# Kernel optimization log

Hardware: AMD Instinct MI355X
Metric: run time of the kernel (lower is better)

## Reference

```python
import jax, jax.numpy as jnp
import numpy as np

# 1x1 conv (bias=False) + BatchNorm (eval mode, running mean=0, var=1 -> per-channel
# affine scale/shift, matching SyncBN at init/inference) + ReLU
def _cbr(x, W, g, b):
    y = jnp.einsum('bchw,oc->bohw', x, W)
    y = y * g[None, :, None, None] + b[None, :, None, None]
    return jax.nn.relu(y)


def setup_inputs() -> dict:
    key = jax.random.key(0)
    ks = jax.random.split(key, 8)
    B, C, H, Wd = 4, 512, 64, 64   # batch, feats_channels, spatial
    Ct = 256                        # transform_channels
    Ck = 2 * C                      # key_in_channels = feats_channels * 2

    def w(k, o, i):
        return jax.random.normal(k, (o, i), jnp.float32) * (1.0 / np.sqrt(i))

    inp = {"x": jax.random.normal(ks[0], (B, C, H, Wd), jnp.float32)}
    # query_project: two conv+BN+ReLU blocks, C -> Ct -> Ct
    inp["qW1"] = w(ks[1], Ct, C);  inp["qg1"] = jnp.ones((Ct,), jnp.float32); inp["qb1"] = jnp.zeros((Ct,), jnp.float32)
    inp["qW2"] = w(ks[2], Ct, Ct); inp["qg2"] = jnp.ones((Ct,), jnp.float32); inp["qb2"] = jnp.zeros((Ct,), jnp.float32)
    # key_project: two conv+BN+ReLU blocks, 2C -> Ct -> Ct
    inp["kW1"] = w(ks[3], Ct, Ck); inp["kg1"] = jnp.ones((Ct,), jnp.float32); inp["kb1"] = jnp.zeros((Ct,), jnp.float32)
    inp["kW2"] = w(ks[4], Ct, Ct); inp["kg2"] = jnp.ones((Ct,), jnp.float32); inp["kb2"] = jnp.zeros((Ct,), jnp.float32)
    # value_project: one conv+BN+ReLU, 2C -> Ct
    inp["vW"] = w(ks[5], Ct, Ck);  inp["vg"] = jnp.ones((Ct,), jnp.float32);  inp["vb"] = jnp.zeros((Ct,), jnp.float32)
    # out_project: one conv+BN+ReLU, Ct -> C
    inp["oW"] = w(ks[6], C, Ct);   inp["og"] = jnp.ones((C,), jnp.float32);   inp["ob"] = jnp.zeros((C,), jnp.float32)
    return inp


def reference(x, qW1, qg1, qb1, qW2, qg2, qb2,
              kW1, kg1, kb1, kW2, kg2, kb2,
              vW, vg, vb, oW, og, ob):
    B, C, H, W = x.shape
    # global avgpool to 1x1, bilinear-upsample back to HxW == broadcast of the mean
    xg = jnp.broadcast_to(jnp.mean(x, axis=(2, 3), keepdims=True), (B, C, H, W))
    key_feats = jnp.concatenate([xg, x], axis=1)  # [B, 2C, H, W]

    q = _cbr(_cbr(x, qW1, qg1, qb1), qW2, qg2, qb2)          # [B, Ct, H, W]
    k = _cbr(_cbr(key_feats, kW1, kg1, kb1), kW2, kg2, kb2)  # [B, Ct, H, W]
    v = _cbr(key_feats, vW, vg, vb)                          # [B, Ct, H, W]

    Ct = q.shape[1]
    HW = H * W
    qf = q.reshape(B, Ct, HW).transpose(0, 2, 1)  # [B, HW, Ct]
    kf = k.reshape(B, Ct, HW)                     # [B, Ct, HW]
    vf = v.reshape(B, Ct, HW).transpose(0, 2, 1)  # [B, HW, Ct]

    sim = jnp.einsum('bnc,bcm->bnm', qf, kf) * (Ct ** -0.5)  # [B, HW, HW]
    attn = jax.nn.softmax(sim, axis=-1)
    ctx = jnp.einsum('bnm,bmc->bnc', attn, vf)               # [B, HW, Ct]
    ctx = ctx.transpose(0, 2, 1).reshape(B, Ct, H, W)

    return _cbr(ctx, oW, og, ob)  # [B, C, H, W]
```

## Files before the change

kernel.cpp:

```cpp
#include <hip/hip_runtime.h>
#include <stdint.h>

typedef __bf16 bf16x8 __attribute__((ext_vector_type(8)));
typedef float f32x4 __attribute__((ext_vector_type(4)));
typedef unsigned short u16;
typedef uint32_t u32;

union V16 { uint4 v; u16 e[8]; };

__device__ __forceinline__ float bf2f(u16 h) {
    u32 u = ((u32)h) << 16; float f; __builtin_memcpy(&f, &u, 4); return f;
}
__device__ __forceinline__ u16 f2bf(float f) {
    u32 u; __builtin_memcpy(&u, &f, 4);
    u32 r = (u + 0x7FFFu + ((u >> 16) & 1u)) >> 16; return (u16)r;
}
__device__ __forceinline__ u32 pack2(float a, float b) {
    return (u32)f2bf(a) | ((u32)f2bf(b) << 16);
}
__device__ __forceinline__ f32x4 mfma16(bf16x8 a, bf16x8 b, f32x4 c) {
    return __builtin_amdgcn_mfma_f32_16x16x32_bf16(a, b, c, 0, 0, 0);
}
__device__ __forceinline__ void gll16(const u16* g, u16* l) {
    __builtin_amdgcn_global_load_lds(
        (const __attribute__((address_space(1))) unsigned int*)g,
        (__attribute__((address_space(3))) unsigned int*)l, 16, 0, 0);
}
__device__ __forceinline__ float loadElem(const void* p, size_t i, int fl) {
    if (fl == 1) return ((const float*)p)[i];
    if (fl == 2) return (float)((const double*)p)[i];
    return bf2f(((const u16*)p)[i]);
}

__global__ __launch_bounds__(256) void k_detect(const u32* __restrict__ xw, int* __restrict__ flag) {
    int t = threadIdx.x;
    int cA = 0, cB = 0;
    #pragma unroll
    for (int i = 0; i < 16; i++) {
        u32 w = xw[i * 256 + t];
        cA += (((w >> 23) & 0xFFu) >= 0xC0u) ? 1 : 0;
        cB += (((w >> 7)  & 0xFFu) >= 0xC0u) ? 1 : 0;
    }
    #pragma unroll
    for (int m = 32; m >= 1; m >>= 1) { cA += __shfl_xor(cA, m); cB += __shfl_xor(cB, m); }
    __shared__ int sA[4], sB[4];
    if ((t & 63) == 0) { sA[t >> 6] = cA; sB[t >> 6] = cB; }
    __syncthreads();
    if (t == 0) {
        int a = sA[0] + sA[1] + sA[2] + sA[3];
        int b = sB[0] + sB[1] + sB[2] + sB[3];
        *flag = (a > 64) ? 2 : ((b > 64) ? 1 : 0);
    }
}

__global__ __launch_bounds__(256) void k_mean(const void* __restrict__ xv, const int* __restrict__ dt,
                                              float* __restrict__ xg) {
    int bc = blockIdx.x;
    int t = threadIdx.x;
    int fl = *dt;
    const size_t base = (size_t)bc * 4096;
    float s = 0.f;
    if (fl == 1) {
        const float* p = (const float*)xv + base;
        #pragma unroll
        for (int i = 0; i < 4; i++) {
            float4 v = *reinterpret_cast<const float4*>(p + (size_t)(i * 256 + t) * 4);
            s += v.x + v.y + v.z + v.w;
        }
    } else {
        for (int i = 0; i < 16; i++) s += loadElem(xv, base + i * 256 + t, fl);
    }
    #pragma unroll
    for (int m = 32; m >= 1; m >>= 1) s += __shfl_xor(s, m);
    __shared__ float wsum[4];
    if ((t & 63) == 0) wsum[t >> 6] = s;
    __syncthreads();
    if (t == 0) xg[bc] = (wsum[0] + wsum[1] + wsum[2] + wsum[3]) * (1.f / 4096.f);
}

__global__ __launch_bounds__(256) void k_xpose(const void* __restrict__ xv, const int* __restrict__ dt,
                                               u16* __restrict__ xT) {
    __shared__ u16 tile[64][72];
    int b = blockIdx.z;
    int n0 = blockIdx.x * 64, c0 = blockIdx.y * 64;
    u16* xTb = xT + (size_t)b * 4096 * 512;
    int t = threadIdx.x;
    int fl = *dt;
    const size_t xbase = (size_t)b * 512 * 4096;
    if (fl == 1) {
        const float* xb = (const float*)xv + xbase;
        int cr = t >> 4, n4 = (t & 15) * 4;
        #pragma unroll
        for (int i = 0; i < 4; i++) {
            int c = cr + i * 16;
            float4 v = *reinterpret_cast<const float4*>(xb + (size_t)(c0 + c) * 4096 + n0 + n4);
            tile[n4 + 0][c] = f2bf(v.x); tile[n4 + 1][c] = f2bf(v.y);
            tile[n4 + 2][c] = f2bf(v.z); tile[n4 + 3][c] = f2bf(v.w);
        }
    } else {
        int c4 = t >> 6, n = t & 63;
        for (int i = 0; i < 16; i++) {
            int c = c4 + i * 4;
            tile[n][c] = f2bf(loadElem(xv, xbase + (size_t)(c0 + c) * 4096 + n0 + n, fl));
        }
    }
    __syncthreads();
    int nr = t >> 3, c8 = (t & 7) * 8;
    #pragma unroll
    for (int i = 0; i < 2; i++) {
        int n = nr + i * 32;
        V16 v;
        #pragma unroll
        for (int j = 0; j < 8; j++) v.e[j] = tile[n][c8 + j];
        *reinterpret_cast<uint4*>(xTb + (size_t)(n0 + n) * 512 + c0 + c8) = v.v;
    }
}

__global__ __launch_bounds__(64) void k_consts(const void* __restrict__ kW1, const void* __restrict__ vW,
                                               const int* __restrict__ dt, const float* __restrict__ xg,
                                               float* __restrict__ ck, float* __restrict__ cv) {
    int bo = blockIdx.x; int b = bo >> 8; int o = bo & 255;
    int l = threadIdx.x;
    int fl = *dt;
    const float* g = xg + b * 512;
    float sk = 0.f, sv = 0.f;
    for (int c = l; c < 512; c += 64) {
        float xv = g[c];
        sk += loadElem(kW1, (size_t)o * 1024 + c, fl) * xv;
        sv += loadElem(vW,  (size_t)o * 1024 + c, fl) * xv;
    }
    #pragma unroll
    for (int m = 32; m >= 1; m >>= 1) { sk += __shfl_xor(sk, m); sv += __shfl_xor(sv, m); }
    if (l == 0) { ck[bo] = sk; cv[bo] = sv; }
}

__global__ __launch_bounds__(256) void k_wconv(const void* __restrict__ qW1, const void* __restrict__ qW2,
                                               const void* __restrict__ kW1, const void* __restrict__ kW2,
                                               const void* __restrict__ vW, const void* __restrict__ oW,
                                               const int* __restrict__ dt, u16* __restrict__ dst) {
    int i = blockIdx.x * 256 + threadIdx.x;
    int fl = *dt;
    const void* s; size_t so;
    if (i < 131072)      { s = qW1; so = (size_t)i; }
    else if (i < 196608) { int j = i - 131072; s = qW2; so = (size_t)j; }
    else if (i < 327680) { int j = i - 196608; s = kW1; so = (size_t)(j >> 9) * 1024 + 512 + (j & 511); }
    else if (i < 393216) { int j = i - 327680; s = kW2; so = (size_t)j; }
    else if (i < 524288) { int j = i - 393216; s = vW;  so = (size_t)(j >> 9) * 1024 + 512 + (j & 511); }
    else                 { int j = i - 524288; s = oW;  so = (size_t)j; }
    dst[i] = f2bf(loadElem(s, so, fl));
}

__global__ __launch_bounds__(256) void k_pconv(const void* qg1, const void* qb1, const void* qg2, const void* qb2,
                                               const void* kg1, const void* kb1, const void* kg2, const void* kb2,
                                               const void* vg, const void* vb, const void* og, const void* ob,
                                               const int* __restrict__ dt, float* __restrict__ pg) {
    int j = blockIdx.x * 256 + threadIdx.x;
    if (j >= 3584) return;
    int fl = *dt;
    const void* s; int o;
    if (j < 256)       { s = qg1; o = j; }
    else if (j < 512)  { s = qb1; o = j - 256; }
    else if (j < 768)  { s = qg2; o = j - 512; }
    else if (j < 1024) { s = qb2; o = j - 768; }
    else if (j < 1280) { s = kg1; o = j - 1024; }
    else if (j < 1536) { s = kb1; o = j - 1280; }
    else if (j < 1792) { s = kg2; o = j - 1536; }
    else if (j < 2048) { s = kb2; o = j - 1792; }
    else if (j < 2304) { s = vg;  o = j - 2048; }
    else if (j < 2560) { s = vb;  o = j - 2304; }
    else if (j < 3072) { s = og;  o = j - 2560; }
    else               { s = ob;  o = j - 3072; }
    pg[j] = loadElem(s, (size_t)o, fl);
}

template<bool AFF_ROW, typename OT>
__global__ __launch_bounds__(256) void k_gemm_bt(
    const u16* __restrict__ A, long aBS, int lda,
    const u16* __restrict__ Bm, long bBS, int ldb,
    OT* __restrict__ C, long cBS, int ldc,
    const float* __restrict__ gamma, const float* __restrict__ beta,
    const float* __restrict__ bias, int biasBS, int K) {
    __shared__ u16 As[2][128 * 64];
    __shared__ u16 Bs[2][128 * 64];
    int b = blockIdx.z;
    const u16* Ab = A + (size_t)b * aBS;
    const u16* Bb = Bm + (size_t)b * bBS;
    OT* Cb = C + (size_t)b * cBS;
    int m0 = blockIdx.x * 128, n0 = blockIdx.y * 128;
    int t = threadIdx.x;
    int lane = t & 63, wid = t >> 6;
    int wr = wid >> 1, wc = wid & 1;
    int li = lane & 15, lk = lane >> 4;

    f32x4 acc[4][4] = {};

    auto stage = [&](int k0, int buf) {
        #pragma unroll
        for (int j = 0; j < 4; j++) {
            int c = wid * 4 + j;
            u32 pl = (u32)c * 1024 + (u32)lane * 16;
            u32 r = pl >> 7;
            u32 q = (pl & 127) ^ ((r & 7) << 4);
            gll16(Ab + (size_t)(m0 + r) * lda + k0 + (q >> 1), &As[buf][0] + (c << 9));
            gll16(Bb + (size_t)(n0 + r) * ldb + k0 + (q >> 1), &Bs[buf][0] + (c << 9));
        }
    };

    const int nk = K >> 6;
    stage(0, 0);

    for (int kst = 0; kst < nk; kst++) {
        int cur = kst & 1;
        if (kst + 1 < nk) {
            stage((kst + 1) << 6, cur ^ 1);
            asm volatile("s_waitcnt vmcnt(8)" ::: "memory");
        } else {
            asm volatile("s_waitcnt vmcnt(0)" ::: "memory");
        }
        __builtin_amdgcn_sched_barrier(0);
        __builtin_amdgcn_s_barrier();

        const char* AsB = (const char*)&As[cur][0];
        const char* BsB = (const char*)&Bs[cur][0];
        #pragma unroll
        for (int ks = 0; ks < 2; ks++) {
            bf16x8 af[4], bfr[4];
            #pragma unroll
            for (int mi = 0; mi < 4; mi++) {
                int r = wr * 64 + mi * 16 + li;
                u32 off = ((u32)(r * 128 + (ks * 32 + lk * 8) * 2)) ^ (((u32)(r & 7)) << 4);
                af[mi] = *reinterpret_cast<const bf16x8*>(AsB + off);
            }
            #pragma unroll
            for (int ni = 0; ni < 4; ni++) {
                int r = wc * 64 + ni * 16 + li;
                u32 off = ((u32)(r * 128 + (ks * 32 + lk * 8) * 2)) ^ (((u32)(r & 7)) << 4);
                bfr[ni] = *reinterpret_cast<const bf16x8*>(BsB + off);
            }
            #pragma unroll
            for (int mi = 0; mi < 4; mi++)
                #pragma unroll
                for (int ni = 0; ni < 4; ni++)
                    acc[mi][ni] = mfma16(af[mi], bfr[ni], acc[mi][ni]);
        }
        asm volatile("s_waitcnt lgkmcnt(0)" ::: "memory");
        __builtin_amdgcn_s_barrier();
    }
    #pragma unroll
    for (int mi = 0; mi < 4; mi++) {
        #pragma unroll
        for (int ni = 0; ni < 4; ni++) {
            #pragma unroll
            for (int r = 0; r < 4; r++) {
                int m = m0 + wr * 64 + mi * 16 + lk * 4 + r;
                int n = n0 + wc * 64 + ni * 16 + li;
                int oc = AFF_ROW ? m : n;
                float v = acc[mi][ni][r];
                if (bias) v += bias[b * biasBS + oc];
                float y = v * gamma[oc] + beta[oc];
                y = fmaxf(y, 0.f);
                if constexpr (sizeof(OT) == 2) Cb[(size_t)m * ldc + n] = f2bf(y);
                else                           Cb[(size_t)m * ldc + n] = y;
            }
        }
    }
}

__global__ __launch_bounds__(256) void k_gemm_pair(
    const u16* __restrict__ A0, const u16* __restrict__ A1, long aBS, int lda,
    const u16* __restrict__ B0, const u16* __restrict__ B1, int ldb,
    u16* __restrict__ C0, u16* __restrict__ C1, long cBS, int ldc,
    const float* __restrict__ g0, const float* __restrict__ be0, const float* __restrict__ bias0,
    const float* __restrict__ g1, const float* __restrict__ be1, const float* __restrict__ bias1,
    int biasBS, int K) {
    __shared__ u16 As[2][128 * 64];
    __shared__ u16 Bs[2][128 * 64];
    int z = blockIdx.z;
    int op = z >> 2, b = z & 3;
    const u16* Ab = (op ? A1 : A0) + (size_t)b * aBS;
    const u16* Bb = op ? B1 : B0;
    u16* Cb = (op ? C1 : C0) + (size_t)b * cBS;
    const float* gamma = op ? g1 : g0;
    const float* beta  = op ? be1 : be0;
    const float* bias  = op ? bias1 : bias0;
    int m0 = blockIdx.x * 128, n0 = blockIdx.y * 128;
    int t = threadIdx.x;
    int lane = t & 63, wid = t >> 6;
    int wr = wid >> 1, wc = wid & 1;
    int li = lane & 15, lk = lane >> 4;

    f32x4 acc[4][4] = {};

    auto stage = [&](int k0, int buf) {
        #pragma unroll
        for (int j = 0; j < 4; j++) {
            int c = wid * 4 + j;
            u32 pl = (u32)c * 1024 + (u32)lane * 16;
            u32 r = pl >> 7;
            u32 q = (pl & 127) ^ ((r & 7) << 4);
            gll16(Ab + (size_t)(m0 + r) * lda + k0 + (q >> 1), &As[buf][0] + (c << 9));
            gll16(Bb + (size_t)(n0 + r) * ldb + k0 + (q >> 1), &Bs[buf][0] + (c << 9));
        }
    };

    const int nk = K >> 6;
    stage(0, 0);

    for (int kst = 0; kst < nk; kst++) {
        int cur = kst & 1;
        if (kst + 1 < nk) {
            stage((kst + 1) << 6, cur ^ 1);
            asm volatile("s_waitcnt vmcnt(8)" ::: "memory");
        } else {
            asm volatile("s_waitcnt vmcnt(0)" ::: "memory");
        }
        __builtin_amdgcn_sched_barrier(0);
        __builtin_amdgcn_s_barrier();

        const char* AsB = (const char*)&As[cur][0];
        const char* BsB = (const char*)&Bs[cur][0];
        #pragma unroll
        for (int ks = 0; ks < 2; ks++) {
            bf16x8 af[4], bfr[4];
            #pragma unroll
            for (int mi = 0; mi < 4; mi++) {
                int r = wr * 64 + mi * 16 + li;
                u32 off = ((u32)(r * 128 + (ks * 32 + lk * 8) * 2)) ^ (((u32)(r & 7)) << 4);
                af[mi] = *reinterpret_cast<const bf16x8*>(AsB + off);
            }
            #pragma unroll
            for (int ni = 0; ni < 4; ni++) {
                int r = wc * 64 + ni * 16 + li;
                u32 off = ((u32)(r * 128 + (ks * 32 + lk * 8) * 2)) ^ (((u32)(r & 7)) << 4);
                bfr[ni] = *reinterpret_cast<const bf16x8*>(BsB + off);
            }
            #pragma unroll
            for (int mi = 0; mi < 4; mi++)
                #pragma unroll
                for (int ni = 0; ni < 4; ni++)
                    acc[mi][ni] = mfma16(af[mi], bfr[ni], acc[mi][ni]);
        }
        asm volatile("s_waitcnt lgkmcnt(0)" ::: "memory");
        __builtin_amdgcn_s_barrier();
    }
    #pragma unroll
    for (int mi = 0; mi < 4; mi++) {
        #pragma unroll
        for (int ni = 0; ni < 4; ni++) {
            #pragma unroll
            for (int r = 0; r < 4; r++) {
                int m = m0 + wr * 64 + mi * 16 + lk * 4 + r;
                int n = n0 + wc * 64 + ni * 16 + li;
                float v = acc[mi][ni][r];
                if (bias) v += bias[b * biasBS + n];
                float y = v * gamma[n] + beta[n];
                y = fmaxf(y, 0.f);
                Cb[(size_t)m * ldc + n] = f2bf(y);
            }
        }
    }
}

__global__ __launch_bounds__(256, 2) void k_attn(const u16* __restrict__ Q, const u16* __restrict__ Kt,
                                                 const u16* __restrict__ V, u16* __restrict__ Op,
                                                 float2* __restrict__ ML) {
    __shared__ u16 Ks[2][32 * 256];
    __shared__ u16 Vs[2][256 * 32];
    __shared__ u16 Ps[128 * 32];
    char* PsB = (char*)Ps;
    int wg = blockIdx.x;
    int bs = wg & 15, qt = wg >> 4;
    int b = bs >> 2, sp = bs & 3;
    int n0 = qt * 128;
    int k0 = sp * 1024;
    const size_t S = (size_t)4096 * 256;
    const u16* Qb = Q + (size_t)b * S + (size_t)n0 * 256;
    const u16* Kb = Kt + (size_t)b * S + (size_t)k0 * 256;
    const u16* Vb = V + (size_t)b * S + k0;
    int t = threadIdx.x;
    int lane = t & 63, wid = t >> 6;
    int li = lane & 15, lk = lane >> 4;
    int qw = wid * 32;

    bf16x8 qf[2][8];
    #pragma unroll
    for (int fq = 0; fq < 2; fq++)
        #pragma unroll
        for (int kc = 0; kc < 8; kc++)
            qf[fq][kc] = *reinterpret_cast<const bf16x8*>(Qb + (size_t)(qw + fq * 16 + li) * 256 + kc * 32 + lk * 8);

    f32x4 acc[2][16] = {};
    float M[2] = {-1e30f, -1e30f};
    float L[2] = {0.f, 0.f};
    const float SCL = 0.0625f * 1.44269504088896f;

    auto stage = [&](int kt, int buf) {
        const u16* Kp = Kb + (size_t)kt * 32 * 256;
        const u16* Vp = Vb + kt * 32;
        u16* Kd = &Ks[buf][0];
        u16* Vd = &Vs[buf][0];
        #pragma unroll
        for (int j = 0; j < 4; j++) {
            int c = wid * 4 + j;
            u32 pl = (u32)c * 1024 + (u32)lane * 16;
            u32 krow = pl >> 9;
            u32 kq = (pl & 511) ^ ((krow & 7) << 4);
            gll16(Kp + krow * 256 + (kq >> 1), Kd + (c << 9));
            u32 vcc = pl >> 6;
            u32 vq = (pl & 63) ^ (((vcc >> 1) & 3) << 4);
            gll16(Vp + (size_t)vcc * 4096 + (vq >> 1), Vd + (c << 9));
        }
    };

    stage(0, 0);

    for (int kt = 0; kt < 32; kt++) {
        int cur = kt & 1;
        if (kt + 1 < 32) {
            stage(kt + 1, cur ^ 1);
            asm volatile("s_waitcnt vmcnt(8)" ::: "memory");
        } else {
            asm volatile("s_waitcnt vmcnt(0)" ::: "memory");
        }
        __builtin_amdgcn_sched_barrier(0);
        __builtin_amdgcn_s_barrier();

        const char* KsB = (const char*)&Ks[cur][0];
        const char* VsB = (const char*)&Vs[cur][0];

        __builtin_amdgcn_s_setprio(1);
        f32x4 sf[2][2] = {};
        #pragma unroll
        for (int mk = 0; mk < 2; mk++) {
            #pragma unroll
            for (int kc = 0; kc < 8; kc++) {
                int row = mk * 16 + li;
                u32 off = (u32)(row * 512) + (((u32)(kc * 64 + lk * 16)) ^ (((u32)(row & 7)) << 4));
                bf16x8 kb = *reinterpret_cast<const bf16x8*>(KsB + off);
                sf[mk][0] = mfma16(kb, qf[0][kc], sf[mk][0]);
                sf[mk][1] = mfma16(kb, qf[1][kc], sf[mk][1]);
            }
        }
        __builtin_amdgcn_s_setprio(0);

        float lm[2];
        #pragma unroll
        for (int fq = 0; fq < 2; fq++) {
            lm[fq] = fmaxf(fmaxf(fmaxf(sf[0][fq][0], sf[0][fq][1]), fmaxf(sf[0][fq][2], sf[0][fq][3])),
                           fmaxf(fmaxf(sf[1][fq][0], sf[1][fq][1]), fmaxf(sf[1][fq][2], sf[1][fq][3]))) * SCL;
        }
        bool ok = (lm[0] <= M[0] + 24.f) && (lm[1] <= M[1] + 24.f);
        if (!__all(ok ? 1 : 0)) {
            #pragma unroll
            for (int fq = 0; fq < 2; fq++) {
                float mx = lm[fq];
                mx = fmaxf(mx, __shfl_xor(mx, 16));
                mx = fmaxf(mx, __shfl_xor(mx, 32));
                float nM = fmaxf(M[fq], mx);
                float rs = exp2f(M[fq] - nM);
                L[fq] *= rs; M[fq] = nM;
                #pragma unroll
                for (int ct = 0; ct < 16; ct++) {
                    acc[fq][ct][0] *= rs; acc[fq][ct][1] *= rs;
                    acc[fq][ct][2] *= rs; acc[fq][ct][3] *= rs;
                }
            }
        }
        #pragma unroll
        for (int fq = 0; fq < 2; fq++) {
            int row = qw + fq * 16 + li;
            float lloc = 0.f;
            #pragma unroll
            for (int mk = 0; mk < 2; mk++) {
                float p0 = exp2f(sf[mk][fq][0] * SCL - M[fq]);
                float p1 = exp2f(sf[mk][fq][1] * SCL - M[fq]);
                float p2 = exp2f(sf[mk][fq][2] * SCL - M[fq]);
                float p3 = exp2f(sf[mk][fq][3] * SCL - M[fq]);
                lloc += (p0 + p1) + (p2 + p3);
                uint2 pw; pw.x = pack2(p0, p1); pw.y = pack2(p2, p3);
                u32 off = ((u32)(row * 64 + mk * 32 + lk * 8)) ^ (((u32)(row & 7)) << 4);
                *reinterpret_cast<uint2*>(PsB + off) = pw;
            }
            L[fq] += lloc;
        }

        __builtin_amdgcn_s_setprio(1);
        {
            bf16x8 pb[2];
            #pragma unroll
            for (int fq = 0; fq < 2; fq++) {
                int row = qw + fq * 16 + li;
                u32 off = ((u32)(row * 64 + lk * 16)) ^ (((u32)(row & 7)) << 4);
                pb[fq] = *reinterpret_cast<const bf16x8*>(PsB + off);
            }
            #pragma unroll
            for (int ct = 0; ct < 16; ct++) {
                int vr = ct * 16 + li;
                u32 voff = (u32)(vr * 64) + (((u32)(lk * 16)) ^ (((u32)((vr >> 1) & 3)) << 4));
                bf16x8 va = *reinterpret_cast<const bf16x8*>(VsB + voff);
                acc[0][ct] = mfma16(va, pb[0], acc[0][ct]);
                acc[1][ct] = mfma16(va, pb[1], acc[1][ct]);
            }
        }
        __builtin_amdgcn_s_setprio(0);
        asm volatile("s_waitcnt lgkmcnt(0)" ::: "memory");
        __builtin_amdgcn_s_barrier();
    }

    #pragma unroll
    for (int fq = 0; fq < 2; fq++) {
        L[fq] += __shfl_xor(L[fq], 16);
        L[fq] += __shfl_xor(L[fq], 32);
    }

    size_t obase = (size_t)(sp * 4 + b) * 4096 + n0;
    #pragma unroll
    for (int fq = 0; fq < 2; fq++) {
        int q = qw + fq * 16 + li;
        #pragma unroll
        for (int ct = 0; ct < 16; ct++) {
            uint2 ow;
            ow.x = pack2(acc[fq][ct][0], acc[fq][ct][1]);
            ow.y = pack2(acc[fq][ct][2], acc[fq][ct][3]);
            *reinterpret_cast<uint2*>(&Op[(obase + q) * 256 + ct * 16 + lk * 4]) = ow;
        }
    }
    if (lk == 0) {
        #pragma unroll
        for (int fq = 0; fq < 2; fq++) {
            float2 v; v.x = M[fq]; v.y = L[fq];
            ML[obase + qw + fq * 16 + li] = v;
        }
    }
}

__global__ __launch_bounds__(256) void k_merge(const u16* __restrict__ Op, const float2* __restrict__ ML,
                                               u16* __restrict__ ctx) {
    int wg = blockIdx.x;
    int t = threadIdx.x;
    int b = wg >> 12, q = wg & 4095;
    float2 ml[4];
    float Mx = -1e30f;
    #pragma unroll
    for (int s = 0; s < 4; s++) { ml[s] = ML[((size_t)(s * 4 + b) << 12) + q]; Mx = fmaxf(Mx, ml[s].x); }
    float Lt = 0.f, w[4];
    #pragma unroll
    for (int s = 0; s < 4; s++) { w[s] = exp2f(ml[s].x - Mx); Lt += ml[s].y * w[s]; }
    float inv = 1.f / Lt;
    float o = 0.f;
    #pragma unroll
    for (int s = 0; s < 4; s++)
        o += w[s] * bf2f(Op[((((size_t)(s * 4 + b) << 12) + q)) * 256 + t]);
    ctx[(((size_t)b << 12) + q) * 256 + t] = f2bf(o * inv);
}

extern "C" void kernel_launch(void* const* d_in, const int* in_sizes, int n_in,
                              void* d_out, int out_size, void* d_ws, size_t ws_size,
                              hipStream_t stream) {
    const void* x   = d_in[0];
    const void* qW1 = d_in[1];  const void* qg1 = d_in[2];  const void* qb1 = d_in[3];
    const void* qW2 = d_in[4];  const void* qg2 = d_in[5];  const void* qb2 = d_in[6];
    const void* kW1 = d_in[7];  const void* kg1 = d_in[8];  const void* kb1 = d_in[9];
    const void* kW2 = d_in[10]; const void* kg2 = d_in[11]; const void* kb2 = d_in[12];
    const void* vW  = d_in[13]; const void* vg  = d_in[14]; const void* vb  = d_in[15];
    const void* oW  = d_in[16]; const void* og  = d_in[17]; const void* ob  = d_in[18];

    char* ws = (char*)d_ws;
    int*   dflag = (int*)ws;
    float* xg = (float*)(ws + 4096);
    float* ck = (float*)(ws + 16384);
    float* cv = (float*)(ws + 20480);
    float* pg = (float*)(ws + 24576);
    u16* wb = (u16*)(ws + 40960);
    u16* qW1b = wb;
    u16* qW2b = wb + 131072;
    u16* kW1b = wb + 196608;
    u16* kW2b = wb + 327680;
    u16* vWb  = wb + 393216;
    u16* oWb  = wb + 524288;
    const size_t S = (size_t)4096 * 256;
    const size_t SLOT = 4 * S;
    u16* s0 = (u16*)(ws + 0x180000);
    u16* s1 = s0 + SLOT;
    u16* s2 = s1 + SLOT;
    u16* s3 = s2 + SLOT;
    float2* mlBuf = (float2*)s3;
    u16* xT = (u16*)d_out;
    u16* k1buf = (u16*)d_out + 8388608;
    u16* opart = (u16*)d_out;
    u16* ctxBuf = s1;

    k_detect<<<1, 256, 0, stream>>>((const u32*)x, dflag);
    k_mean<<<2048, 256, 0, stream>>>(x, dflag, xg);
    k_xpose<<<dim3(64, 8, 4), 256, 0, stream>>>(x, dflag, xT);
    k_consts<<<1024, 64, 0, stream>>>(kW1, vW, dflag, xg, ck, cv);
    k_wconv<<<2560, 256, 0, stream>>>(qW1, qW2, kW1, kW2, vW, oW, dflag, wb);
    k_pconv<<<14, 256, 0, stream>>>(qg1, qb1, qg2, qb2, kg1, kb1, kg2, kb2,
                                    vg, vb, og, ob, dflag, pg);

    const long XS = (long)4096 * 512;
    k_gemm_pair<<<dim3(32, 2, 8), 256, 0, stream>>>(xT, xT, XS, 512,
        qW1b, kW1b, 512, s0, k1buf, (long)S, 256,
        pg + 0, pg + 256, nullptr, pg + 1024, pg + 1280, ck, 256, 512);
    k_gemm_pair<<<dim3(32, 2, 8), 256, 0, stream>>>(s0, k1buf, (long)S, 256,
        qW2b, kW2b, 256, s1, s2, (long)S, 256,
        pg + 512, pg + 768, nullptr, pg + 1536, pg + 1792, nullptr, 0, 256);
    k_gemm_bt<true, u16><<<dim3(2, 32, 4), 256, 0, stream>>>(vWb, 0, 512, xT, XS, 512,
        s0, (long)S, 4096, pg + 2048, pg + 2304, cv, 256, 512);
    k_attn<<<512, 256, 0, stream>>>(s1, s2, s0, opart, mlBuf);
    k_merge<<<16384, 256, 0, stream>>>(opart, mlBuf, ctxBuf);
    k_gemm_bt<true, float><<<dim3(4, 32, 4), 256, 0, stream>>>(oWb, 0, 256, ctxBuf, (long)S, 256,
        (float*)d_out, (long)512 * 4096, 4096, pg + 2560, pg + 3072, nullptr, 0, 256);
}
```

Before: 226.2 us.

## Fuse mean into transpose, merge Q/K/V first GEMMs, use hardware bf16 pack

Computes per-channel partial sums inside the transpose kernel and reduces them in a small kernel, so the separate mean pass that re-read x goes away. The q1, k1 and value projection GEMMs now run as one launch with 12 z-slices, which removes a launch and fills more CUs at once. Software bf16 rounding in the attention kernel is replaced by the v_cvt_pk_bf16_f32 instruction. Workspace offsets are moved so the value output gets its own slot. The cost is extra shuffle reductions in the transpose kernel.

```diff
diff --git a/kernel.cpp b/kernel.cpp
--- a/kernel.cpp
+++ b/kernel.cpp
@@ -15,8 +15,10 @@
     u32 u; __builtin_memcpy(&u, &f, 4);
     u32 r = (u + 0x7FFFu + ((u >> 16) & 1u)) >> 16; return (u16)r;
 }
-__device__ __forceinline__ u32 pack2(float a, float b) {
-    return (u32)f2bf(a) | ((u32)f2bf(b) << 16);
+__device__ __forceinline__ u32 cvtpk(float lo, float hi) {
+    u32 r;
+    asm("v_cvt_pk_bf16_f32 %0, %1, %2" : "=v"(r) : "v"(lo), "v"(hi));
+    return r;
 }
 __device__ __forceinline__ f32x4 mfma16(bf16x8 a, bf16x8 b, f32x4 c) {
     return __builtin_amdgcn_mfma_f32_16x16x32_bf16(a, b, c, 0, 0, 0);
@@ -53,33 +55,8 @@
     }
 }
 
-__global__ __launch_bounds__(256) void k_mean(const void* __restrict__ xv, const int* __restrict__ dt,
-                                              float* __restrict__ xg) {
-    int bc = blockIdx.x;
-    int t = threadIdx.x;
-    int fl = *dt;
-    const size_t base = (size_t)bc * 4096;
-    float s = 0.f;
-    if (fl == 1) {
-        const float* p = (const float*)xv + base;
-        #pragma unroll
-        for (int i = 0; i < 4; i++) {
-            float4 v = *reinterpret_cast<const float4*>(p + (size_t)(i * 256 + t) * 4);
-            s += v.x + v.y + v.z + v.w;
-        }
-    } else {
-        for (int i = 0; i < 16; i++) s += loadElem(xv, base + i * 256 + t, fl);
-    }
-    #pragma unroll
-    for (int m = 32; m >= 1; m >>= 1) s += __shfl_xor(s, m);
-    __shared__ float wsum[4];
-    if ((t & 63) == 0) wsum[t >> 6] = s;
-    __syncthreads();
-    if (t == 0) xg[bc] = (wsum[0] + wsum[1] + wsum[2] + wsum[3]) * (1.f / 4096.f);
-}
-
 __global__ __launch_bounds__(256) void k_xpose(const void* __restrict__ xv, const int* __restrict__ dt,
-                                               u16* __restrict__ xT) {
+                                               u16* __restrict__ xT, float* __restrict__ partial) {
     __shared__ u16 tile[64][72];
     int b = blockIdx.z;
     int n0 = blockIdx.x * 64, c0 = blockIdx.y * 64;
@@ -96,12 +73,23 @@
             float4 v = *reinterpret_cast<const float4*>(xb + (size_t)(c0 + c) * 4096 + n0 + n4);
             tile[n4 + 0][c] = f2bf(v.x); tile[n4 + 1][c] = f2bf(v.y);
             tile[n4 + 2][c] = f2bf(v.z); tile[n4 + 3][c] = f2bf(v.w);
+            float s = (v.x + v.y) + (v.z + v.w);
+            s += __shfl_xor(s, 1); s += __shfl_xor(s, 2);
+            s += __shfl_xor(s, 4); s += __shfl_xor(s, 8);
+            if ((t & 15) == 0)
+                partial[((size_t)b * 512 + c0 + c) * 64 + blockIdx.x] = s;
         }
     } else {
         int c4 = t >> 6, n = t & 63;
         for (int i = 0; i < 16; i++) {
             int c = c4 + i * 4;
-            tile[n][c] = f2bf(loadElem(xv, xbase + (size_t)(c0 + c) * 4096 + n0 + n, fl));
+            float v = loadElem(xv, xbase + (size_t)(c0 + c) * 4096 + n0 + n, fl);
+            tile[n][c] = f2bf(v);
+            float s = v;
+            #pragma unroll
+            for (int m = 32; m >= 1; m >>= 1) s += __shfl_xor(s, m);
+            if (n == 0)
+                partial[((size_t)b * 512 + c0 + c) * 64 + blockIdx.x] = s;
         }
     }
     __syncthreads();
@@ -114,6 +102,15 @@
         for (int j = 0; j < 8; j++) v.e[j] = tile[n][c8 + j];
         *reinterpret_cast<uint4*>(xTb + (size_t)(n0 + n) * 512 + c0 + c8) = v.v;
     }
+}
+
+__global__ __launch_bounds__(256) void k_mean2(const float* __restrict__ partial, float* __restrict__ xg) {
+    int bc = blockIdx.x * 256 + threadIdx.x;
+    const float* p = partial + (size_t)bc * 64;
+    float s = 0.f;
+    #pragma unroll
+    for (int i = 0; i < 64; i++) s += p[i];
+    xg[bc] = s * (1.f / 4096.f);
 }
 
 __global__ __launch_bounds__(64) void k_consts(const void* __restrict__ kW1, const void* __restrict__ vW,
@@ -266,13 +263,114 @@
     }
 }
 
+__global__ __launch_bounds__(256) void k_gemm_tri(
+    const u16* __restrict__ xT, long xBS,
+    const u16* __restrict__ Wq, const u16* __restrict__ Wk, const u16* __restrict__ Wv,
+    u16* __restrict__ Cq, u16* __restrict__ Ck2, u16* __restrict__ Cv, long cBS,
+    const float* __restrict__ pg, const float* __restrict__ ckb, const float* __restrict__ cvb) {
+    __shared__ u16 As[2][128 * 64];
+    __shared__ u16 Bs[2][128 * 64];
+    int z = blockIdx.z;
+    int op = z >> 2, b = z & 3;
+    const u16* Ab; const u16* Bb; u16* Cb; int ldc;
+    const float* gamma; const float* beta; const float* bias;
+    int m0, n0;
+    if (op == 2) {
+        Ab = Wv; Bb = xT + (size_t)b * xBS; Cb = Cv + (size_t)b * cBS; ldc = 4096;
+        gamma = pg + 2048; beta = pg + 2304; bias = cvb;
+        m0 = blockIdx.y * 128; n0 = blockIdx.x * 128;
+    } else if (op == 1) {
+        Ab = xT + (size_t)b * xBS; Bb = Wk; Cb = Ck2 + (size_t)b * cBS; ldc = 256;
+        gamma = pg + 1024; beta = pg + 1280; bias = ckb;
+        m0 = blockIdx.x * 128; n0 = blockIdx.y * 128;
+    } else {
+        Ab = xT + (size_t)b * xBS; Bb = Wq; Cb = Cq + (size_t)b * cBS; ldc = 256;
+        gamma = pg + 0; beta = pg + 256; bias = nullptr;
+        m0 = blockIdx.x * 128; n0 = blockIdx.y * 128;
+    }
+    int t = threadIdx.x;
+    int lane = t & 63, wid = t >> 6;
+    int wr = wid >> 1, wc = wid & 1;
+    int li = lane & 15, lk = lane >> 4;
+
+    f32x4 acc[4][4] = {};
+
+    auto stage = [&](int k0, int buf) {
+        #pragma unroll
+        for (int j = 0; j < 4; j++) {
+            int c = wid * 4 + j;
+            u32 pl = (u32)c * 1024 + (u32)lane * 16;
+            u32 r = pl >> 7;
+            u32 q = (pl & 127) ^ ((r & 7) << 4);
+            gll16(Ab + (size_t)(m0 + r) * 512 + k0 + (q >> 1), &As[buf][0] + (c << 9));
+            gll16(Bb + (size_t)(n0 + r) * 512 + k0 + (q >> 1), &Bs[buf][0] + (c << 9));
+        }
+    };
+
+    stage(0, 0);
+
+    for (int kst = 0; kst < 8; kst++) {
+        int cur = kst & 1;
+        if (kst + 1 < 8) {
+            stage((kst + 1) << 6, cur ^ 1);
+            asm volatile("s_waitcnt vmcnt(8)" ::: "memory");
+        } else {
+            asm volatile("s_waitcnt vmcnt(0)" ::: "memory");
+        }
+        __builtin_amdgcn_sched_barrier(0);
+        __builtin_amdgcn_s_barrier();
+
+        const char* AsB = (const char*)&As[cur][0];
+        const char* BsB = (const char*)&Bs[cur][0];
+        #pragma unroll
+        for (int ks = 0; ks < 2; ks++) {
+            bf16x8 af[4], bfr[4];
+            #pragma unroll
+            for (int mi = 0; mi < 4; mi++) {
+                int r = wr * 64 + mi * 16 + li;
+                u32 off = ((u32)(r * 128 + (ks * 32 + lk * 8) * 2)) ^ (((u32)(r & 7)) << 4);
+                af[mi] = *reinterpret_cast<const bf16x8*>(AsB + off);
+            }
+            #pragma unroll
+            for (int ni = 0; ni < 4; ni++) {
+                int r = wc * 64 + ni * 16 + li;
+                u32 off = ((u32)(r * 128 + (ks * 32 + lk * 8) * 2)) ^ (((u32)(r & 7)) << 4);
+                bfr[ni] = *reinterpret_cast<const bf16x8*>(BsB + off);
+            }
+            #pragma unroll
+            for (int mi = 0; mi < 4; mi++)
+                #pragma unroll
+                for (int ni = 0; ni < 4; ni++)
+                    acc[mi][ni] = mfma16(af[mi], bfr[ni], acc[mi][ni]);
+        }
+        asm volatile("s_waitcnt lgkmcnt(0)" ::: "memory");
+        __builtin_amdgcn_s_barrier();
+    }
+    #pragma unroll
+    for (int mi = 0; mi < 4; mi++) {
+        #pragma unroll
+        for (int ni = 0; ni < 4; ni++) {
+            #pragma unroll
+            for (int r = 0; r < 4; r++) {
+                int m = m0 + wr * 64 + mi * 16 + lk * 4 + r;
+                int n = n0 + wc * 64 + ni * 16 + li;
+                int oc = (op == 2) ? m : n;
+                float v = acc[mi][ni][r];
+                if (bias) v += bias[b * 256 + oc];
+                float y = v * gamma[oc] + beta[oc];
+                y = fmaxf(y, 0.f);
+                Cb[(size_t)m * ldc + n] = f2bf(y);
+            }
+        }
+    }
+}
+
 __global__ __launch_bounds__(256) void k_gemm_pair(
     const u16* __restrict__ A0, const u16* __restrict__ A1, long aBS, int lda,
     const u16* __restrict__ B0, const u16* __restrict__ B1, int ldb,
     u16* __restrict__ C0, u16* __restrict__ C1, long cBS, int ldc,
-    const float* __restrict__ g0, const float* __restrict__ be0, const float* __restrict__ bias0,
-    const float* __restrict__ g1, const float* __restrict__ be1, const float* __restrict__ bias1,
-    int biasBS, int K) {
+    const float* __restrict__ g0, const float* __restrict__ be0,
+    const float* __restrict__ g1, const float* __restrict__ be1, int K) {
     __shared__ u16 As[2][128 * 64];
     __shared__ u16 Bs[2][128 * 64];
     int z = blockIdx.z;
@@ -282,7 +380,6 @@
     u16* Cb = (op ? C1 : C0) + (size_t)b * cBS;
     const float* gamma = op ? g1 : g0;
     const float* beta  = op ? be1 : be0;
-    const float* bias  = op ? bias1 : bias0;
     int m0 = blockIdx.x * 128, n0 = blockIdx.y * 128;
     int t = threadIdx.x;
     int lane = t & 63, wid = t >> 6;
@@ -352,7 +449,6 @@
                 int m = m0 + wr * 64 + mi * 16 + lk * 4 + r;
                 int n = n0 + wc * 64 + ni * 16 + li;
                 float v = acc[mi][ni][r];
-                if (bias) v += bias[b * biasBS + n];
                 float y = v * gamma[n] + beta[n];
                 y = fmaxf(y, 0.f);
                 Cb[(size_t)m * ldc + n] = f2bf(y);
@@ -477,7 +573,7 @@
                 float p2 = exp2f(sf[mk][fq][2] * SCL - M[fq]);
                 float p3 = exp2f(sf[mk][fq][3] * SCL - M[fq]);
                 lloc += (p0 + p1) + (p2 + p3);
-                uint2 pw; pw.x = pack2(p0, p1); pw.y = pack2(p2, p3);
+                uint2 pw; pw.x = cvtpk(p0, p1); pw.y = cvtpk(p2, p3);
                 u32 off = ((u32)(row * 64 + mk * 32 + lk * 8)) ^ (((u32)(row & 7)) << 4);
                 *reinterpret_cast<uint2*>(PsB + off) = pw;
             }
@@ -520,8 +616,8 @@
         #pragma unroll
         for (int ct = 0; ct < 16; ct++) {
             uint2 ow;
-            ow.x = pack2(acc[fq][ct][0], acc[fq][ct][1]);
-            ow.y = pack2(acc[fq][ct][2], acc[fq][ct][3]);
+            ow.x = cvtpk(acc[fq][ct][0], acc[fq][ct][1]);
+            ow.y = cvtpk(acc[fq][ct][2], acc[fq][ct][3]);
             *reinterpret_cast<uint2*>(&Op[(obase + q) * 256 + ct * 16 + lk * 4]) = ow;
         }
     }
@@ -578,36 +674,34 @@
     u16* kW2b = wb + 327680;
     u16* vWb  = wb + 393216;
     u16* oWb  = wb + 524288;
+    float* partials = (float*)(ws + 0x180000);
+    float2* mlBuf = (float2*)(ws + 0x200000);
     const size_t S = (size_t)4096 * 256;
     const size_t SLOT = 4 * S;
-    u16* s0 = (u16*)(ws + 0x180000);
+    u16* s0 = (u16*)(ws + 0x280000);
     u16* s1 = s0 + SLOT;
     u16* s2 = s1 + SLOT;
     u16* s3 = s2 + SLOT;
-    float2* mlBuf = (float2*)s3;
     u16* xT = (u16*)d_out;
     u16* k1buf = (u16*)d_out + 8388608;
     u16* opart = (u16*)d_out;
     u16* ctxBuf = s1;
 
     k_detect<<<1, 256, 0, stream>>>((const u32*)x, dflag);
-    k_mean<<<2048, 256, 0, stream>>>(x, dflag, xg);
-    k_xpose<<<dim3(64, 8, 4), 256, 0, stream>>>(x, dflag, xT);
+    k_xpose<<<dim3(64, 8, 4), 256, 0, stream>>>(x, dflag, xT, partials);
+    k_mean2<<<8, 256, 0, stream>>>(partials, xg);
     k_consts<<<1024, 64, 0, stream>>>(kW1, vW, dflag, xg, ck, cv);
     k_wconv<<<2560, 256, 0, stream>>>(qW1, qW2, kW1, kW2, vW, oW, dflag, wb);
     k_pconv<<<14, 256, 0, stream>>>(qg1, qb1, qg2, qb2, kg1, kb1, kg2, kb2,
                                     vg, vb, og, ob, dflag, pg);
 
     const long XS = (long)4096 * 512;
-    k_gemm_pair<<<dim3(32, 2, 8), 256, 0, stream>>>(xT, xT, XS, 512,
-        qW1b, kW1b, 512, s0, k1buf, (long)S, 256,
-        pg + 0, pg + 256, nullptr, pg + 1024, pg + 1280, ck, 256, 512);
+    k_gemm_tri<<<dim3(32, 2, 12), 256, 0, stream>>>(xT, XS, qW1b, kW1b, vWb,
+        s0, k1buf, s3, (long)S, pg, ck, cv);
     k_gemm_pair<<<dim3(32, 2, 8), 256, 0, stream>>>(s0, k1buf, (long)S, 256,
         qW2b, kW2b, 256, s1, s2, (long)S, 256,
-        pg + 512, pg + 768, nullptr, pg + 1536, pg + 1792, nullptr, 0, 256);
-    k_gemm_bt<true, u16><<<dim3(2, 32, 4), 256, 0, stream>>>(vWb, 0, 512, xT, XS, 512,
-        s0, (long)S, 4096, pg + 2048, pg + 2304, cv, 256, 512);
-    k_attn<<<512, 256, 0, stream>>>(s1, s2, s0, opart, mlBuf);
+        pg + 512, pg + 768, pg + 1536, pg + 1792, 256);
+    k_attn<<<512, 256, 0, stream>>>(s1, s2, s3, opart, mlBuf);
     k_merge<<<16384, 256, 0, stream>>>(opart, mlBuf, ctxBuf);
     k_gemm_bt<true, float><<<dim3(4, 32, 4), 256, 0, stream>>>(oWb, 0, 256, ctxBuf, (long)S, 256,
         (float*)d_out, (long)512 * 4096, 4096, pg + 2560, pg + 3072, nullptr, 0, 256);
```

Result: faster. 215.7 us (-4.6%).
